# Kernel tuning notes

Hardware: AMD Instinct MI355X
Metric: run time of the kernel (lower is better)

The kernel has to match this reference:

```python
import jax, jax.numpy as jnp
import numpy as np

B = 32
GRID_H, GRID_W = 28, 28
DIM, HEADS, HEAD_DIM = 768, 8, 96
KS_HEADS = [(3, 2), (5, 3), (7, 3)]  # (kernel_size, num_heads) -> 2+3+3 = 8 heads


def setup_inputs() -> dict:
    key = jax.random.key(0)
    ks = jax.random.split(key, 8)
    n = GRID_H * GRID_W + 1  # +1 for CLS token
    inp = {
        "x": jax.random.normal(ks[0], (B, n, DIM), jnp.float32),
        "W_qkv": jax.random.normal(ks[1], (DIM, 3 * DIM), jnp.float32) * 0.02,
        "b_qkv": jnp.zeros((3 * DIM,), jnp.float32),
        "W_out": jax.random.normal(ks[2], (DIM, DIM), jnp.float32) * 0.02,
        "b_out": jnp.zeros((DIM,), jnp.float32),
    }
    for i, (k, nh) in enumerate(KS_HEADS):
        c = nh * HEAD_DIM
        inp[f"conv_w{k}"] = jax.random.normal(ks[3 + i], (c, 1, k, k), jnp.float32) * 0.02
        inp[f"conv_b{k}"] = jnp.zeros((c,), jnp.float32)
    inp["H"] = GRID_H
    inp["W"] = GRID_W
    return inp


def _dwconv(x, w, b, k):
    # depthwise conv, NCHW, 'same' padding for odd k
    out = jax.lax.conv_general_dilated(
        x, w, (1, 1), [(k // 2, k // 2)] * 2,
        feature_group_count=x.shape[1],
        dimension_numbers=("NCHW", "OIHW", "NCHW"))
    return out + b[None, :, None, None]


def _crpe(v_img, conv_params, Hh, Ww):
    # v_img: (b, h, H*W, d) -> channels (h*d) are head-contiguous
    b, h, n, d = v_img.shape
    x = v_img.transpose(0, 1, 3, 2).reshape(b, h * d, Hh, Ww)
    outs, start = [], 0
    for (k, nh), (w, bb) in zip(KS_HEADS, conv_params):
        c = nh * d
        outs.append(_dwconv(x[:, start:start + c], w, bb, k))
        start += c
    x = jnp.concatenate(outs, axis=1)
    return x.reshape(b, h, d, n).transpose(0, 1, 3, 2)


def reference(x, W_qkv, b_qkv, conv_w3, conv_b3, conv_w5, conv_b5,
              conv_w7, conv_b7, W_out, b_out, H, W):
    b, n, dim = x.shape
    h, d = HEADS, HEAD_DIM
    scale = d ** -0.5
    qkv = x @ W_qkv + b_qkv                       # (b, n, 3*dim)
    q, k, v = jnp.split(qkv, 3, axis=-1)

    def to_heads(t):
        return t.reshape(b, n, h, d).transpose(0, 2, 1, 3)  # (b, h, n, d)

    q, k, v = to_heads(q), to_heads(k), to_heads(v)
    k = jax.nn.softmax(k, axis=2)                 # softmax over tokens n
    attn = jnp.einsum('bhnd,bhne->bhde', k, v)    # linear-attention factor (d x d)

    conv_params = [(conv_w3, conv_b3), (conv_w5, conv_b5), (conv_w7, conv_b7)]
    rp_img = _crpe(v[:, :, 1:, :], conv_params, H, W)          # (b, h, H*W, d)
    rp = jnp.concatenate([jnp.zeros((b, h, 1, d), v.dtype), rp_img], axis=2)

    out = jnp.einsum('bhnd,bhde->bhne', q * scale, attn) + q * rp
    out = out.transpose(0, 2, 1, 3).reshape(b, n, dim)
    return out @ W_out + b_out
```

## Files before the change

### kernel.cpp

```cpp
#include <hip/hip_runtime.h>
#include <hip/hip_bf16.h>
#include <math.h>

#define BN    32
#define NTOK  785
#define GH    28
#define GW    28
#define DIM   768
#define QKVD  2304
#define NH    8
#define HD    96
#define MROWS (BN*NTOK)
#define NS    4
#define NPC   197

typedef __hip_bfloat16 bf16;
typedef unsigned short ushort_t;
typedef short s16x8 __attribute__((ext_vector_type(8)));
typedef float f32x4 __attribute__((ext_vector_type(4)));

__device__ __forceinline__ void gl2lds16(const void* g, void* l) {
    __builtin_amdgcn_global_load_lds(
        (__attribute__((address_space(1))) void*)const_cast<void*>(g),
        (__attribute__((address_space(3))) void*)l, 16, 0, 0);
}

__device__ __forceinline__ ushort_t f2bf(float f) {
    bf16 h = __float2bfloat16(f);
    return *(ushort_t*)&h;
}

__device__ __forceinline__ s16x8 cvt8(const float* p) {
    float4 a = *(const float4*)p;
    float4 b = *(const float4*)(p + 4);
    union { s16x8 v; __hip_bfloat162 h[4]; } r;
    r.h[0] = __float22bfloat162_rn(make_float2(a.x, a.y));
    r.h[1] = __float22bfloat162_rn(make_float2(a.z, a.w));
    r.h[2] = __float22bfloat162_rn(make_float2(b.x, b.y));
    r.h[3] = __float22bfloat162_rn(make_float2(b.z, b.w));
    return r.v;
}

__global__ __launch_bounds__(256)
void f32_to_bf16_kernel(const float* __restrict__ in, ushort_t* __restrict__ out,
                        int n8) {
    int i = blockIdx.x * 256 + threadIdx.x;
    if (i >= n8) return;
    const float4* p = (const float4*)(in + (size_t)i * 8);
    float4 a = p[0], b = p[1];
    union { s16x8 v; __hip_bfloat162 h[4]; } r;
    r.h[0] = __float22bfloat162_rn(make_float2(a.x, a.y));
    r.h[1] = __float22bfloat162_rn(make_float2(a.z, a.w));
    r.h[2] = __float22bfloat162_rn(make_float2(b.x, b.y));
    r.h[3] = __float22bfloat162_rn(make_float2(b.z, b.w));
    *(s16x8*)(out + (size_t)i * 8) = r.v;
}

__global__ __launch_bounds__(256)
void transpose_bf16_kernel(const float* __restrict__ W, ushort_t* __restrict__ Wt,
                           int R, int C) {
    __shared__ float tile[32][33];
    int c0 = blockIdx.x * 32, r0 = blockIdx.y * 32;
    int tx = threadIdx.x, ty = threadIdx.y;
    #pragma unroll
    for (int i = 0; i < 4; ++i)
        tile[ty + i * 8][tx] = W[(size_t)(r0 + ty + i * 8) * C + c0 + tx];
    __syncthreads();
    #pragma unroll
    for (int i = 0; i < 4; ++i)
        Wt[(size_t)(c0 + ty + i * 8) * R + r0 + tx] = f2bf(tile[tx][ty + i * 8]);
}

__global__ __launch_bounds__(256)
void gemm_qkv_mfma(const ushort_t* __restrict__ A, const ushort_t* __restrict__ Bt,
                   const float* __restrict__ bias,
                   ushort_t* __restrict__ q, ushort_t* __restrict__ kk,
                   ushort_t* __restrict__ v) {
    const int M = MROWS, K = DIM;
    __shared__ ushort_t Asm[128 * 32];
    __shared__ ushort_t Bsm[128 * 32];
    const int tid  = threadIdx.x;
    const int wave = tid >> 6;
    const int lane = tid & 63;
    const int row0 = blockIdx.y * 128;
    const int col0 = blockIdx.x * 128;
    const int wm = wave >> 1, wn = wave & 1;
    const int q4 = lane >> 4, l15 = lane & 15;
    const int slotg = (lane & 3) ^ ((lane >> 3) & 3);
    const int swz   = (l15 >> 1) & 3;

    f32x4 acc[4][4];
    #pragma unroll
    for (int i = 0; i < 4; ++i)
        #pragma unroll
        for (int j = 0; j < 4; ++j) acc[i][j] = (f32x4){0.f, 0.f, 0.f, 0.f};

    for (int kt = 0; kt < K; kt += 32) {
        #pragma unroll
        for (int r = 0; r < 2; ++r) {
            int seg = r * 4 + wave;
            int rit = seg * 16 + (lane >> 2);
            int grow = min(row0 + rit, M - 1);
            const ushort_t* gp = A + (size_t)grow * K + kt + slotg * 8;
            gl2lds16(gp, &Asm[seg * 512]);
        }
        #pragma unroll
        for (int r = 0; r < 2; ++r) {
            int seg = r * 4 + wave;
            int nit = seg * 16 + (lane >> 2);
            const ushort_t* gp = Bt + (size_t)(col0 + nit) * K + kt + slotg * 8;
            gl2lds16(gp, &Bsm[seg * 512]);
        }
        __syncthreads();
        s16x8 af[4], bfr[4];
        #pragma unroll
        for (int mi = 0; mi < 4; ++mi)
            af[mi] = *(const s16x8*)&Asm[(wm * 64 + mi * 16 + l15) * 32
                                         + ((q4 ^ swz) * 8)];
        #pragma unroll
        for (int ni = 0; ni < 4; ++ni)
            bfr[ni] = *(const s16x8*)&Bsm[(wn * 64 + ni * 16 + l15) * 32
                                          + ((q4 ^ swz) * 8)];
        #pragma unroll
        for (int mi = 0; mi < 4; ++mi)
            #pragma unroll
            for (int ni = 0; ni < 4; ++ni)
                acc[mi][ni] = __builtin_amdgcn_mfma_f32_16x16x32_bf16(
                    af[mi], bfr[ni], acc[mi][ni], 0, 0, 0);
        __syncthreads();
    }
    int colbase = col0 + wn * 64;
    int seg = colbase / DIM;
    int csub = colbase - seg * DIM;
    ushort_t* outp = (seg == 0) ? q : (seg == 1) ? kk : v;
    #pragma unroll
    for (int mi = 0; mi < 4; ++mi) {
        #pragma unroll
        for (int ni = 0; ni < 4; ++ni) {
            int gcol = colbase + ni * 16 + l15;
            int col  = csub + ni * 16 + l15;
            float bb = bias[gcol];
            #pragma unroll
            for (int j = 0; j < 4; ++j) {
                int row = row0 + wm * 64 + mi * 16 + q4 * 4 + j;
                if (row < M)
                    outp[(size_t)row * DIM + col] = f2bf(acc[mi][ni][j] + bb);
            }
        }
    }
}

__global__ __launch_bounds__(256)
void gemm_out_mfma(const ushort_t* __restrict__ A, const ushort_t* __restrict__ Bt,
                   const float* __restrict__ bias, float* __restrict__ C) {
    const int M = MROWS, N = DIM, K = DIM;
    __shared__ ushort_t Asm[128 * 32];
    __shared__ ushort_t Bsm[128 * 32];
    const int tid  = threadIdx.x;
    const int wave = tid >> 6;
    const int lane = tid & 63;
    const int row0 = blockIdx.y * 128;
    const int col0 = blockIdx.x * 128;
    const int wm = wave >> 1, wn = wave & 1;
    const int q4 = lane >> 4, l15 = lane & 15;
    const int slotg = (lane & 3) ^ ((lane >> 3) & 3);
    const int swz   = (l15 >> 1) & 3;

    f32x4 acc[4][4];
    #pragma unroll
    for (int i = 0; i < 4; ++i)
        #pragma unroll
        for (int j = 0; j < 4; ++j) acc[i][j] = (f32x4){0.f, 0.f, 0.f, 0.f};

    for (int kt = 0; kt < K; kt += 32) {
        #pragma unroll
        for (int r = 0; r < 2; ++r) {
            int seg = r * 4 + wave;
            int rit = seg * 16 + (lane >> 2);
            int grow = min(row0 + rit, M - 1);
            const ushort_t* gp = A + (size_t)grow * K + kt + slotg * 8;
            gl2lds16(gp, &Asm[seg * 512]);
        }
        #pragma unroll
        for (int r = 0; r < 2; ++r) {
            int seg = r * 4 + wave;
            int nit = seg * 16 + (lane >> 2);
            const ushort_t* gp = Bt + (size_t)(col0 + nit) * K + kt + slotg * 8;
            gl2lds16(gp, &Bsm[seg * 512]);
        }
        __syncthreads();
        s16x8 af[4], bfr[4];
        #pragma unroll
        for (int mi = 0; mi < 4; ++mi)
            af[mi] = *(const s16x8*)&Asm[(wm * 64 + mi * 16 + l15) * 32
                                         + ((q4 ^ swz) * 8)];
        #pragma unroll
        for (int ni = 0; ni < 4; ++ni)
            bfr[ni] = *(const s16x8*)&Bsm[(wn * 64 + ni * 16 + l15) * 32
                                          + ((q4 ^ swz) * 8)];
        #pragma unroll
        for (int mi = 0; mi < 4; ++mi)
            #pragma unroll
            for (int ni = 0; ni < 4; ++ni)
                acc[mi][ni] = __builtin_amdgcn_mfma_f32_16x16x32_bf16(
                    af[mi], bfr[ni], acc[mi][ni], 0, 0, 0);
        __syncthreads();
    }
    #pragma unroll
    for (int mi = 0; mi < 4; ++mi) {
        #pragma unroll
        for (int ni = 0; ni < 4; ++ni) {
            int col = col0 + wn * 64 + ni * 16 + l15;
            float bb = bias[col];
            #pragma unroll
            for (int j = 0; j < 4; ++j) {
                int row = row0 + wm * 64 + mi * 16 + q4 * 4 + j;
                if (row < M)
                    C[(size_t)row * N + col] = acc[mi][ni][j] + bb;
            }
        }
    }
}

__global__ __launch_bounds__(256)
void softmax_stats_kernel(const bf16* __restrict__ k,
                          float* __restrict__ stat_m, float* __restrict__ stat_is) {
    int b = blockIdx.y;
    int c = blockIdx.x * 64 + threadIdx.x;
    int ty = threadIdx.y;
    const bf16* base = k + (size_t)b * NTOK * DIM + c;
    float m = -1e30f, s = 0.f;
    for (int n = ty; n < NTOK; n += 4) {
        float kv = __bfloat162float(base[(size_t)n * DIM]);
        float nm = fmaxf(m, kv);
        s = s * __expf(m - nm) + __expf(kv - nm);
        m = nm;
    }
    __shared__ float sm[4][64], ss[4][64];
    sm[ty][threadIdx.x] = m; ss[ty][threadIdx.x] = s;
    __syncthreads();
    if (ty == 0) {
        float M = sm[0][threadIdx.x];
        #pragma unroll
        for (int i = 1; i < 4; ++i) M = fmaxf(M, sm[i][threadIdx.x]);
        float S = 0.f;
        #pragma unroll
        for (int i = 0; i < 4; ++i) S += ss[i][threadIdx.x] * __expf(sm[i][threadIdx.x] - M);
        stat_m[b * DIM + c] = M;
        stat_is[b * DIM + c] = 1.f / S;
    }
}

__global__ __launch_bounds__(256)
void attn_kernel(const bf16* __restrict__ k, const bf16* __restrict__ v,
                 const float* __restrict__ stat_m,
                 float* __restrict__ attn_part) {
    const int h = blockIdx.x, b = blockIdx.y, ns = blockIdx.z;
    const int t = threadIdx.x;
    const int wave = t >> 6, lane = t & 63;
    const int q4 = lane >> 4, l15 = lane & 15;
    const int wd = wave >> 1, we = wave & 1;
    __shared__ float ekT[96][36];
    __shared__ float vT[96][36];
    __shared__ float smM[96];
    if (t < 96) smM[t] = stat_m[b * DIM + h * HD + t];
    __syncthreads();

    f32x4 acc[3][3];
    #pragma unroll
    for (int i = 0; i < 3; ++i)
        #pragma unroll
        for (int j = 0; j < 3; ++j) acc[i][j] = (f32x4){0.f, 0.f, 0.f, 0.f};

    const bf16* kbase = k + (size_t)b * NTOK * DIM + h * HD;
    const bf16* vbase = v + (size_t)b * NTOK * DIM + h * HD;
    const int nlo = ns * NPC;
    const int nhi = min(NTOK, nlo + NPC);
    const int tl = t >> 3;
    const int cg = (t & 7) * 12;
    for (int n0 = nlo; n0 < nhi; n0 += 32) {
        const int n = n0 + tl;
        if (n < nhi) {
            #pragma unroll
            for (int j = 0; j < 6; ++j) {
                float2 kf = __bfloat1622float2(
                    *(const __hip_bfloat162*)&kbase[(size_t)n * DIM + cg + 2 * j]);
                float2 vf = __bfloat1622float2(
                    *(const __hip_bfloat162*)&vbase[(size_t)n * DIM + cg + 2 * j]);
                ekT[cg + 2 * j][tl]     = __expf(kf.x - smM[cg + 2 * j]);
                ekT[cg + 2 * j + 1][tl] = __expf(kf.y - smM[cg + 2 * j + 1]);
                vT[cg + 2 * j][tl]      = vf.x;
                vT[cg + 2 * j + 1][tl]  = vf.y;
            }
        } else {
            #pragma unroll
            for (int j = 0; j < 12; ++j) {
                ekT[cg + j][tl] = 0.f;
                vT[cg + j][tl]  = 0.f;
            }
        }
        __syncthreads();
        s16x8 af[3], bfr[3];
        #pragma unroll
        for (int i = 0; i < 3; ++i)
            af[i] = cvt8(&ekT[wd * 48 + i * 16 + l15][q4 * 8]);
        #pragma unroll
        for (int i = 0; i < 3; ++i)
            bfr[i] = cvt8(&vT[we * 48 + i * 16 + l15][q4 * 8]);
        #pragma unroll
        for (int i = 0; i < 3; ++i)
            #pragma unroll
            for (int j = 0; j < 3; ++j)
                acc[i][j] = __builtin_amdgcn_mfma_f32_16x16x32_bf16(
                    af[i], bfr[j], acc[i][j], 0, 0, 0);
        __syncthreads();
    }
    float* abase = attn_part + (size_t)ns * BN * NH * HD * HD
                 + (size_t)(b * NH + h) * HD * HD;
    #pragma unroll
    for (int i = 0; i < 3; ++i)
        #pragma unroll
        for (int j = 0; j < 3; ++j)
            #pragma unroll
            for (int r = 0; r < 4; ++r)
                abase[(size_t)(wd * 48 + i * 16 + q4 * 4 + r) * HD
                      + we * 48 + j * 16 + l15] = acc[i][j][r];
}

__global__ __launch_bounds__(256)
void attn_reduce_kernel(const float* __restrict__ part,
                        const float* __restrict__ stat_is,
                        float* __restrict__ attn) {
    const int TOT4 = BN * NH * HD * HD / 4;
    int i = blockIdx.x * 256 + threadIdx.x;
    if (i >= TOT4) return;
    size_t base = (size_t)i * 4;
    int bh = (int)(base / (HD * HD));
    int d  = (int)((base / HD) % HD);
    float is = stat_is[(bh >> 3) * DIM + (bh & 7) * HD + d];
    const size_t PSZ = (size_t)BN * NH * HD * HD;
    float4 s = *(const float4*)&part[base];
    float4 p1 = *(const float4*)&part[PSZ + base];
    float4 p2 = *(const float4*)&part[2 * PSZ + base];
    float4 p3 = *(const float4*)&part[3 * PSZ + base];
    s.x = (s.x + p1.x + p2.x + p3.x) * is;
    s.y = (s.y + p1.y + p2.y + p3.y) * is;
    s.z = (s.z + p1.z + p2.z + p3.z) * is;
    s.w = (s.w + p1.w + p2.w + p3.w) * is;
    *(float4*)&attn[base] = s;
}

#define CRS 1104

template<int KS>
__device__ __forceinline__ void crpe_conv32(const ushort_t* __restrict__ vimg,
                                            const float* __restrict__ wsm,
                                            float b0, float b1,
                                            ushort_t* __restrict__ ob,
                                            int p, int yl, int y) {
    constexpr int R = KS / 2;
    const float* wA = wsm + (2 * p) * KS * KS;
    const float* wB = wA + KS * KS;
    #pragma unroll
    for (int xo = 0; xo < 28; xo += 7) {
        float a0[7], a1[7];
        #pragma unroll
        for (int u = 0; u < 7; ++u) { a0[u] = b0; a1[u] = b1; }
        #pragma unroll
        for (int ky = 0; ky < KS; ++ky) {
            const ushort_t* rp = vimg + (yl + ky - R + 3) * CRS
                                      + (xo - R + 3) * 32 + 2 * p;
            float2 seg[6 + KS];
            #pragma unroll
            for (int i = 0; i < 6 + KS; ++i)
                seg[i] = __bfloat1622float2(*(const __hip_bfloat162*)(rp + i * 32));
            #pragma unroll
            for (int kx = 0; kx < KS; ++kx) {
                float wa = wA[ky * KS + kx];
                float wb = wB[ky * KS + kx];
                #pragma unroll
                for (int u = 0; u < 7; ++u) {
                    a0[u] = fmaf(wa, seg[u + kx].x, a0[u]);
                    a1[u] = fmaf(wb, seg[u + kx].y, a1[u]);
                }
            }
        }
        #pragma unroll
        for (int u = 0; u < 7; ++u)
            *(__hip_bfloat162*)&ob[(size_t)(1 + y * GW + xo + u) * DIM + 2 * p] =
                __float22bfloat162_rn(make_float2(a0[u], a1[u]));
    }
}

__global__ __launch_bounds__(256)
void crpe_lds_kernel(const ushort_t* __restrict__ v,
                     const float* __restrict__ w3, const float* __restrict__ b3,
                     const float* __restrict__ w5, const float* __restrict__ b5,
                     const float* __restrict__ w7, const float* __restrict__ b7,
                     ushort_t* __restrict__ o) {
    __shared__ ushort_t vimg[20 * CRS];
    __shared__ float    wsm[32 * 49];
    const int cg  = blockIdx.x;
    const int hf  = blockIdx.y;
    const int b   = blockIdx.z;
    const int tid = threadIdx.x;
    const int c0  = cg * 32;

    const float* wsrc; const float* bsrc; int ks;
    if (c0 < 192)      { wsrc = w3 + c0 * 9;          bsrc = b3 + c0;         ks = 3; }
    else if (c0 < 480) { wsrc = w5 + (c0 - 192) * 25; bsrc = b5 + (c0 - 192); ks = 5; }
    else               { wsrc = w7 + (c0 - 480) * 49; bsrc = b7 + (c0 - 480); ks = 7; }
    const int ksq = ks * ks;

    const int zr0 = hf ? 17 : 0;
    for (int idx = tid; idx < 3 * 138; idx += 256) {
        int rr = idx / 138, cc = idx - rr * 138;
        *(s16x8*)&vimg[(zr0 + rr) * CRS + cc * 8] = (s16x8){0,0,0,0,0,0,0,0};
    }
    for (int idx = tid; idx < 17 * 24; idx += 256) {
        int vr = idx / 24, cc = idx - vr * 24;
        int ly = hf ? vr : vr + 3;
        int ch = (cc < 12) ? cc : (112 + cc);
        *(s16x8*)&vimg[ly * CRS + ch * 8] = (s16x8){0,0,0,0,0,0,0,0};
    }
    for (int idx = tid; idx < 32 * ksq; idx += 256)
        wsm[idx] = wsrc[idx];
    const ushort_t* vb = v + (size_t)b * NTOK * DIM + c0;
    const int gy0 = hf ? 11 : 0;
    for (int idx = tid; idx < 17 * 28 * 4; idx += 256) {
        int vr = idx / 112, rem = idx - vr * 112;
        int px = rem >> 2, c8 = rem & 3;
        int gy = gy0 + vr;
        int ly = hf ? vr : vr + 3;
        *(s16x8*)&vimg[ly * CRS + (px + 3) * 32 + c8 * 8] =
            *(const s16x8*)(vb + (size_t)(1 + gy * GW + px) * DIM + c8 * 8);
    }
    ushort_t* ob = o + (size_t)b * NTOK * DIM + c0;
    if (hf == 0 && tid < 32) ob[tid] = 0;
    __syncthreads();

    const int p  = tid & 15;
    const int yl = tid >> 4;
    if (yl >= 14) return;
    const int y = hf * 14 + yl;
    float bb0 = bsrc[2 * p], bb1 = bsrc[2 * p + 1];
    if (ks == 3)      crpe_conv32<3>(vimg, wsm, bb0, bb1, ob, p, yl, y);
    else if (ks == 5) crpe_conv32<5>(vimg, wsm, bb0, bb1, ob, p, yl, y);
    else              crpe_conv32<7>(vimg, wsm, bb0, bb1, ob, p, yl, y);
}

__global__ __launch_bounds__(256)
void combine_kernel(const ushort_t* __restrict__ q, const float* __restrict__ attn,
                    ushort_t* __restrict__ o) {
    const int h = blockIdx.x, b = blockIdx.z;
    const int n0 = blockIdx.y * 64;
    const int t = threadIdx.x;
    const int wave = t >> 6, lane = t & 63;
    const int q4 = lane >> 4, l15 = lane & 15;
    __shared__ ushort_t qs[64][104];
    __shared__ ushort_t atT[96][104];

    const ushort_t* qbase = q + (size_t)b * NTOK * DIM + h * HD;
    #pragma unroll
    for (int i = 0; i < 3; ++i) {
        int idx = t + i * 256;
        int rr = idx / 12, c8 = idx % 12;
        int n = n0 + rr;
        s16x8 val = (s16x8){0,0,0,0,0,0,0,0};
        if (n < NTOK) val = *(const s16x8*)(qbase + (size_t)n * DIM + c8 * 8);
        *(s16x8*)&qs[rr][c8 * 8] = val;
    }
    const float* abase = attn + (size_t)(b * NH + h) * HD * HD;
    #pragma unroll
    for (int i = 0; i < 36; ++i) {
        int idx = t + i * 256;
        int d = idx / 96, e = idx % 96;
        atT[e][d] = f2bf(abase[idx]);
    }
    __syncthreads();

    f32x4 acc[6];
    #pragma unroll
    for (int i = 0; i < 6; ++i) acc[i] = (f32x4){0.f, 0.f, 0.f, 0.f};
    #pragma unroll
    for (int ks = 0; ks < 3; ++ks) {
        s16x8 aq = *(const s16x8*)&qs[wave * 16 + l15][ks * 32 + q4 * 8];
        #pragma unroll
        for (int et = 0; et < 6; ++et) {
            s16x8 bfrg = *(const s16x8*)&atT[et * 16 + l15][ks * 32 + q4 * 8];
            acc[et] = __builtin_amdgcn_mfma_f32_16x16x32_bf16(
                aq, bfrg, acc[et], 0, 0, 0);
        }
    }

    const float scale = 0.10206207261596575f;
    ushort_t* obase = o + (size_t)b * NTOK * DIM + h * HD;
    #pragma unroll
    for (int et = 0; et < 6; ++et) {
        int e = et * 16 + l15;
        #pragma unroll
        for (int r = 0; r < 4; ++r) {
            int rr = wave * 16 + q4 * 4 + r;
            int n = n0 + rr;
            if (n >= NTOK) continue;
            size_t oa = (size_t)n * DIM + e;
            float rp = __bfloat162float(*(const bf16*)&obase[oa]);
            float qv = __bfloat162float(*(const bf16*)&qs[rr][e]);
            obase[oa] = f2bf(scale * acc[et][r] + qv * rp);
        }
    }
}

extern "C" void kernel_launch(void* const* d_in, const int* in_sizes, int n_in,
                              void* d_out, int out_size, void* d_ws, size_t ws_size,
                              hipStream_t stream) {
    const float* x     = (const float*)d_in[0];
    const float* W_qkv = (const float*)d_in[1];
    const float* b_qkv = (const float*)d_in[2];
    const float* W_out = (const float*)d_in[3];
    const float* b_out = (const float*)d_in[4];
    const float* w3    = (const float*)d_in[5];
    const float* cb3   = (const float*)d_in[6];
    const float* w5    = (const float*)d_in[7];
    const float* cb5   = (const float*)d_in[8];
    const float* w7    = (const float*)d_in[9];
    const float* cb7   = (const float*)d_in[10];
    float* out = (float*)d_out;

    ushort_t* q = (ushort_t*)d_ws;
    ushort_t* k = q + (size_t)MROWS * DIM;
    ushort_t* v = k + (size_t)MROWS * DIM;
    float* attn    = (float*)(v + (size_t)MROWS * DIM);
    float* stat_m  = attn + (size_t)BN * NH * HD * HD;
    float* stat_is = stat_m + (size_t)BN * DIM;
    ushort_t* Wqkvt = (ushort_t*)(stat_is + (size_t)BN * DIM);
    ushort_t* Wot   = Wqkvt + (size_t)QKVD * DIM;
    ushort_t* o = k;

    ushort_t* xb = (ushort_t*)d_out;
    float* attn_part = (float*)d_out + (size_t)MROWS * DIM / 2;

    transpose_bf16_kernel<<<dim3(QKVD / 32, DIM / 32), dim3(32, 8), 0, stream>>>(
        W_qkv, Wqkvt, DIM, QKVD);
    transpose_bf16_kernel<<<dim3(DIM / 32, DIM / 32), dim3(32, 8), 0, stream>>>(
        W_out, Wot, DIM, DIM);
    {
        int n8 = MROWS * DIM / 8;
        f32_to_bf16_kernel<<<dim3((n8 + 255) / 256), 256, 0, stream>>>(x, xb, n8);
    }
    gemm_qkv_mfma<<<dim3(QKVD / 128, (MROWS + 127) / 128), 256, 0, stream>>>(
        xb, Wqkvt, b_qkv, q, k, v);
    softmax_stats_kernel<<<dim3(12, BN), dim3(64, 4), 0, stream>>>(
        (const bf16*)k, stat_m, stat_is);
    attn_kernel<<<dim3(NH, BN, NS), 256, 0, stream>>>(
        (const bf16*)k, (const bf16*)v, stat_m, attn_part);
    {
        int tot4 = BN * NH * HD * HD / 4;
        attn_reduce_kernel<<<dim3((tot4 + 255) / 256), 256, 0, stream>>>(
            attn_part, stat_is, attn);
    }
    crpe_lds_kernel<<<dim3(24, 2, BN), 256, 0, stream>>>(
        v, w3, cb3, w5, cb5, w7, cb7, o);
    combine_kernel<<<dim3(NH, 13, BN), 256, 0, stream>>>(
        q, attn, o);
    gemm_out_mfma<<<dim3(DIM / 128, (MROWS + 127) / 128), 256, 0, stream>>>(
        o, Wot, b_out, out);
}
```

Baseline: 564.2 us.

## Double GEMM K-tile to 64 with 8-way swizzle; vectorize two-pass softmax stats

Both MFMA GEMMs now stage 64-wide K tiles in LDS with a new XOR swizzle over eight 16-byte slots. Each barrier pair now covers two MFMA sub-steps, which halves the number of synchronizations per output tile at the cost of double the LDS per block. The softmax statistics kernel is rewritten to read 8 bf16 values per thread with vector loads and to use a two-pass max-then-sum scheme. This replaces the per-element online rescaling exps, but the k tensor is read twice.

```diff
diff --git a/kernel.cpp b/kernel.cpp
--- a/kernel.cpp
+++ b/kernel.cpp
@@ -28,6 +28,10 @@
 __device__ __forceinline__ ushort_t f2bf(float f) {
     bf16 h = __float2bfloat16(f);
     return *(ushort_t*)&h;
+}
+
+__device__ __forceinline__ float bf2f(ushort_t u) {
+    return __bfloat162float(*(const bf16*)&u);
 }
 
 __device__ __forceinline__ s16x8 cvt8(const float* p) {
@@ -77,8 +81,8 @@
                    ushort_t* __restrict__ q, ushort_t* __restrict__ kk,
                    ushort_t* __restrict__ v) {
     const int M = MROWS, K = DIM;
-    __shared__ ushort_t Asm[128 * 32];
-    __shared__ ushort_t Bsm[128 * 32];
+    __shared__ ushort_t Asm[128 * 64];
+    __shared__ ushort_t Bsm[128 * 64];
     const int tid  = threadIdx.x;
     const int wave = tid >> 6;
     const int lane = tid & 63;
@@ -86,8 +90,8 @@
     const int col0 = blockIdx.x * 128;
     const int wm = wave >> 1, wn = wave & 1;
     const int q4 = lane >> 4, l15 = lane & 15;
-    const int slotg = (lane & 3) ^ ((lane >> 3) & 3);
-    const int swz   = (l15 >> 1) & 3;
+    const int l8 = lane >> 3;
+    const int sg = ((lane & 7) ^ l8) * 8;
 
     f32x4 acc[4][4];
     #pragma unroll
@@ -95,38 +99,37 @@
         #pragma unroll
         for (int j = 0; j < 4; ++j) acc[i][j] = (f32x4){0.f, 0.f, 0.f, 0.f};
 
-    for (int kt = 0; kt < K; kt += 32) {
-        #pragma unroll
-        for (int r = 0; r < 2; ++r) {
-            int seg = r * 4 + wave;
-            int rit = seg * 16 + (lane >> 2);
-            int grow = min(row0 + rit, M - 1);
-            const ushort_t* gp = A + (size_t)grow * K + kt + slotg * 8;
-            gl2lds16(gp, &Asm[seg * 512]);
-        }
-        #pragma unroll
-        for (int r = 0; r < 2; ++r) {
-            int seg = r * 4 + wave;
-            int nit = seg * 16 + (lane >> 2);
-            const ushort_t* gp = Bt + (size_t)(col0 + nit) * K + kt + slotg * 8;
-            gl2lds16(gp, &Bsm[seg * 512]);
+    for (int kt = 0; kt < K; kt += 64) {
+        #pragma unroll
+        for (int rr = 0; rr < 4; ++rr) {
+            int lrow = wave * 32 + rr * 8;
+            int grow = min(row0 + lrow + l8, M - 1);
+            gl2lds16(A + (size_t)grow * K + kt + sg, &Asm[lrow * 64]);
+        }
+        #pragma unroll
+        for (int rr = 0; rr < 4; ++rr) {
+            int lrow = wave * 32 + rr * 8;
+            gl2lds16(Bt + (size_t)(col0 + lrow + l8) * K + kt + sg,
+                     &Bsm[lrow * 64]);
         }
         __syncthreads();
-        s16x8 af[4], bfr[4];
-        #pragma unroll
-        for (int mi = 0; mi < 4; ++mi)
-            af[mi] = *(const s16x8*)&Asm[(wm * 64 + mi * 16 + l15) * 32
-                                         + ((q4 ^ swz) * 8)];
-        #pragma unroll
-        for (int ni = 0; ni < 4; ++ni)
-            bfr[ni] = *(const s16x8*)&Bsm[(wn * 64 + ni * 16 + l15) * 32
-                                          + ((q4 ^ swz) * 8)];
-        #pragma unroll
-        for (int mi = 0; mi < 4; ++mi)
+        #pragma unroll
+        for (int kh = 0; kh < 2; ++kh) {
+            const int sl = ((kh * 4 + q4) ^ (l15 & 7)) * 8;
+            s16x8 af[4], bfr[4];
+            #pragma unroll
+            for (int mi = 0; mi < 4; ++mi)
+                af[mi] = *(const s16x8*)&Asm[(wm * 64 + mi * 16 + l15) * 64 + sl];
             #pragma unroll
             for (int ni = 0; ni < 4; ++ni)
-                acc[mi][ni] = __builtin_amdgcn_mfma_f32_16x16x32_bf16(
-                    af[mi], bfr[ni], acc[mi][ni], 0, 0, 0);
+                bfr[ni] = *(const s16x8*)&Bsm[(wn * 64 + ni * 16 + l15) * 64 + sl];
+            #pragma unroll
+            for (int mi = 0; mi < 4; ++mi)
+                #pragma unroll
+                for (int ni = 0; ni < 4; ++ni)
+                    acc[mi][ni] = __builtin_amdgcn_mfma_f32_16x16x32_bf16(
+                        af[mi], bfr[ni], acc[mi][ni], 0, 0, 0);
+        }
         __syncthreads();
     }
     int colbase = col0 + wn * 64;
@@ -154,8 +157,8 @@
 void gemm_out_mfma(const ushort_t* __restrict__ A, const ushort_t* __restrict__ Bt,
                    const float* __restrict__ bias, float* __restrict__ C) {
     const int M = MROWS, N = DIM, K = DIM;
-    __shared__ ushort_t Asm[128 * 32];
-    __shared__ ushort_t Bsm[128 * 32];
+    __shared__ ushort_t Asm[128 * 64];
+    __shared__ ushort_t Bsm[128 * 64];
     const int tid  = threadIdx.x;
     const int wave = tid >> 6;
     const int lane = tid & 63;
@@ -163,8 +166,8 @@
     const int col0 = blockIdx.x * 128;
     const int wm = wave >> 1, wn = wave & 1;
     const int q4 = lane >> 4, l15 = lane & 15;
-    const int slotg = (lane & 3) ^ ((lane >> 3) & 3);
-    const int swz   = (l15 >> 1) & 3;
+    const int l8 = lane >> 3;
+    const int sg = ((lane & 7) ^ l8) * 8;
 
     f32x4 acc[4][4];
     #pragma unroll
@@ -172,38 +175,37 @@
         #pragma unroll
         for (int j = 0; j < 4; ++j) acc[i][j] = (f32x4){0.f, 0.f, 0.f, 0.f};
 
-    for (int kt = 0; kt < K; kt += 32) {
-        #pragma unroll
-        for (int r = 0; r < 2; ++r) {
-            int seg = r * 4 + wave;
-            int rit = seg * 16 + (lane >> 2);
-            int grow = min(row0 + rit, M - 1);
-            const ushort_t* gp = A + (size_t)grow * K + kt + slotg * 8;
-            gl2lds16(gp, &Asm[seg * 512]);
-        }
-        #pragma unroll
-        for (int r = 0; r < 2; ++r) {
-            int seg = r * 4 + wave;
-            int nit = seg * 16 + (lane >> 2);
-            const ushort_t* gp = Bt + (size_t)(col0 + nit) * K + kt + slotg * 8;
-            gl2lds16(gp, &Bsm[seg * 512]);
+    for (int kt = 0; kt < K; kt += 64) {
+        #pragma unroll
+        for (int rr = 0; rr < 4; ++rr) {
+            int lrow = wave * 32 + rr * 8;
+            int grow = min(row0 + lrow + l8, M - 1);
+            gl2lds16(A + (size_t)grow * K + kt + sg, &Asm[lrow * 64]);
+        }
+        #pragma unroll
+        for (int rr = 0; rr < 4; ++rr) {
+            int lrow = wave * 32 + rr * 8;
+            gl2lds16(Bt + (size_t)(col0 + lrow + l8) * K + kt + sg,
+                     &Bsm[lrow * 64]);
         }
         __syncthreads();
-        s16x8 af[4], bfr[4];
-        #pragma unroll
-        for (int mi = 0; mi < 4; ++mi)
-            af[mi] = *(const s16x8*)&Asm[(wm * 64 + mi * 16 + l15) * 32
-                                         + ((q4 ^ swz) * 8)];
-        #pragma unroll
-        for (int ni = 0; ni < 4; ++ni)
-            bfr[ni] = *(const s16x8*)&Bsm[(wn * 64 + ni * 16 + l15) * 32
-                                          + ((q4 ^ swz) * 8)];
-        #pragma unroll
-        for (int mi = 0; mi < 4; ++mi)
+        #pragma unroll
+        for (int kh = 0; kh < 2; ++kh) {
+            const int sl = ((kh * 4 + q4) ^ (l15 & 7)) * 8;
+            s16x8 af[4], bfr[4];
+            #pragma unroll
+            for (int mi = 0; mi < 4; ++mi)
+                af[mi] = *(const s16x8*)&Asm[(wm * 64 + mi * 16 + l15) * 64 + sl];
             #pragma unroll
             for (int ni = 0; ni < 4; ++ni)
-                acc[mi][ni] = __builtin_amdgcn_mfma_f32_16x16x32_bf16(
-                    af[mi], bfr[ni], acc[mi][ni], 0, 0, 0);
+                bfr[ni] = *(const s16x8*)&Bsm[(wn * 64 + ni * 16 + l15) * 64 + sl];
+            #pragma unroll
+            for (int mi = 0; mi < 4; ++mi)
+                #pragma unroll
+                for (int ni = 0; ni < 4; ++ni)
+                    acc[mi][ni] = __builtin_amdgcn_mfma_f32_16x16x32_bf16(
+                        af[mi], bfr[ni], acc[mi][ni], 0, 0, 0);
+        }
         __syncthreads();
     }
     #pragma unroll
@@ -223,31 +225,55 @@
 }
 
 __global__ __launch_bounds__(256)
-void softmax_stats_kernel(const bf16* __restrict__ k,
+void softmax_stats_kernel(const ushort_t* __restrict__ k,
                           float* __restrict__ stat_m, float* __restrict__ stat_is) {
-    int b = blockIdx.y;
-    int c = blockIdx.x * 64 + threadIdx.x;
-    int ty = threadIdx.y;
-    const bf16* base = k + (size_t)b * NTOK * DIM + c;
-    float m = -1e30f, s = 0.f;
-    for (int n = ty; n < NTOK; n += 4) {
-        float kv = __bfloat162float(base[(size_t)n * DIM]);
-        float nm = fmaxf(m, kv);
-        s = s * __expf(m - nm) + __expf(kv - nm);
-        m = nm;
-    }
-    __shared__ float sm[4][64], ss[4][64];
-    sm[ty][threadIdx.x] = m; ss[ty][threadIdx.x] = s;
-    __syncthreads();
-    if (ty == 0) {
-        float M = sm[0][threadIdx.x];
-        #pragma unroll
-        for (int i = 1; i < 4; ++i) M = fmaxf(M, sm[i][threadIdx.x]);
+    const int b  = blockIdx.y;
+    const int c0 = blockIdx.x * 64;
+    const int tid = threadIdx.x;
+    const int c8 = tid & 7, tg = tid >> 3;
+    __shared__ float red[32][64];
+    __shared__ float smB[64];
+    const ushort_t* base = k + (size_t)b * NTOK * DIM + c0 + c8 * 8;
+
+    float mx[8];
+    #pragma unroll
+    for (int j = 0; j < 8; ++j) mx[j] = -1e30f;
+    for (int n = tg; n < NTOK; n += 32) {
+        union { s16x8 v; ushort_t u[8]; } kv;
+        kv.v = *(const s16x8*)(base + (size_t)n * DIM);
+        #pragma unroll
+        for (int j = 0; j < 8; ++j) mx[j] = fmaxf(mx[j], bf2f(kv.u[j]));
+    }
+    #pragma unroll
+    for (int j = 0; j < 8; ++j) red[tg][c8 * 8 + j] = mx[j];
+    __syncthreads();
+    if (tid < 64) {
+        float M = red[0][tid];
+        #pragma unroll
+        for (int i = 1; i < 32; ++i) M = fmaxf(M, red[i][tid]);
+        smB[tid] = M;
+    }
+    __syncthreads();
+
+    float sm8[8], ss[8];
+    #pragma unroll
+    for (int j = 0; j < 8; ++j) { sm8[j] = smB[c8 * 8 + j]; ss[j] = 0.f; }
+    for (int n = tg; n < NTOK; n += 32) {
+        union { s16x8 v; ushort_t u[8]; } kv;
+        kv.v = *(const s16x8*)(base + (size_t)n * DIM);
+        #pragma unroll
+        for (int j = 0; j < 8; ++j) ss[j] += __expf(bf2f(kv.u[j]) - sm8[j]);
+    }
+    __syncthreads();
+    #pragma unroll
+    for (int j = 0; j < 8; ++j) red[tg][c8 * 8 + j] = ss[j];
+    __syncthreads();
+    if (tid < 64) {
         float S = 0.f;
         #pragma unroll
-        for (int i = 0; i < 4; ++i) S += ss[i][threadIdx.x] * __expf(sm[i][threadIdx.x] - M);
-        stat_m[b * DIM + c] = M;
-        stat_is[b * DIM + c] = 1.f / S;
+        for (int i = 0; i < 32; ++i) S += red[i][tid];
+        stat_m[b * DIM + c0 + tid]  = smB[tid];
+        stat_is[b * DIM + c0 + tid] = 1.f / S;
     }
 }
 
@@ -550,8 +576,8 @@
     }
     gemm_qkv_mfma<<<dim3(QKVD / 128, (MROWS + 127) / 128), 256, 0, stream>>>(
         xb, Wqkvt, b_qkv, q, k, v);
-    softmax_stats_kernel<<<dim3(12, BN), dim3(64, 4), 0, stream>>>(
-        (const bf16*)k, stat_m, stat_is);
+    softmax_stats_kernel<<<dim3(12, BN), 256, 0, stream>>>(
+        k, stat_m, stat_is);
     attn_kernel<<<dim3(NH, BN, NS), 256, 0, stream>>>(
         (const bf16*)k, (const bf16*)v, stat_m, attn_part);
     {
```

Measured after the change: 536.0 us. 5.0% less time.
